# Kernel optimization log

Measured on AMD Instinct MI355X. Metric: run time of the kernel, lower is better.

Reference implementation:

```python
import jax, jax.numpy as jnp
import numpy as np

D_MODEL = 1024
NUM_HEADS = 16
DEPTH = D_MODEL // NUM_HEADS
B, S = 2, 2048


def setup_inputs() -> dict:
    key = jax.random.key(0)
    ks = jax.random.split(key, 12)
    scale = 1.0 / np.sqrt(D_MODEL)
    inp = {
        "Q": jax.random.normal(ks[0], (B, S, D_MODEL), jnp.float32),
        "K": jax.random.normal(ks[1], (B, S, D_MODEL), jnp.float32),
        "V": jax.random.normal(ks[2], (B, S, D_MODEL), jnp.float32),
        # causal mask: 1 where attention is disallowed (strictly upper triangular)
        "mask": jnp.triu(jnp.ones((1, 1, S, S), jnp.float32), k=1),
        "Wq": jax.random.normal(ks[3], (D_MODEL, D_MODEL), jnp.float32) * scale,
        "bq": jnp.zeros((D_MODEL,), jnp.float32),
        "Wk": jax.random.normal(ks[4], (D_MODEL, D_MODEL), jnp.float32) * scale,
        "bk": jnp.zeros((D_MODEL,), jnp.float32),
        "Wv": jax.random.normal(ks[5], (D_MODEL, D_MODEL), jnp.float32) * scale,
        "bv": jnp.zeros((D_MODEL,), jnp.float32),
        "Wo": jax.random.normal(ks[6], (D_MODEL, D_MODEL), jnp.float32) * scale,
        "bo": jnp.zeros((D_MODEL,), jnp.float32),
    }
    return inp


def _split_heads(x):
    # [B, S, d_model] -> [B, H, S, depth]
    b, s, _ = x.shape
    return x.reshape(b, s, NUM_HEADS, DEPTH).transpose(0, 2, 1, 3)


def reference(Q, K, V, mask, Wq, bq, Wk, bk, Wv, bv, Wo, bo):
    q = _split_heads(Q @ Wq + bq)  # [B,H,S,depth]
    k = _split_heads(K @ Wk + bk)
    v = _split_heads(V @ Wv + bv)

    scale = 1.0 / jnp.sqrt(jnp.asarray(DEPTH, q.dtype))
    scores = jnp.einsum("bhqd,bhkd->bhqk", q, k) * scale
    scores = scores + mask * (-1e9)
    attn = jax.nn.softmax(scores, axis=-1)  # [B,H,S,S]
    ctx = jnp.einsum("bhqk,bhkd->bhqd", attn, v)

    # combine heads: [B,H,S,depth] -> [B,S,d_model]
    ctx = ctx.transpose(0, 2, 1, 3).reshape(Q.shape[0], -1, D_MODEL)
    out = ctx @ Wo + bo
    return out, attn
```

## Files before the change

kernel.cpp:

```cpp
#include <hip/hip_runtime.h>
#include <hip/hip_bf16.h>
#include <cstdint>
#include <cstddef>


typedef __bf16 bf16x8 __attribute__((ext_vector_type(8)));
typedef float  f32x4  __attribute__((ext_vector_type(4)));
typedef short  short8 __attribute__((ext_vector_type(8)));
typedef unsigned short u16;
typedef unsigned int   u32;

using gas_p = const __attribute__((address_space(1))) void*;
using las_p = __attribute__((address_space(3))) void*;

static __device__ __forceinline__ u16 f2bf(float x) {
    unsigned u = __builtin_bit_cast(unsigned, x);
    u += 0x7FFFu + ((u >> 16) & 1u);
    return (u16)(u >> 16);
}
static __device__ __forceinline__ u32 pk2(float a, float b) {
    return (u32)f2bf(a) | ((u32)f2bf(b) << 16);
}
static __device__ __forceinline__ f32x4 mfma16(bf16x8 a, bf16x8 b, f32x4 c) {
    return __builtin_amdgcn_mfma_f32_16x16x32_bf16(a, b, c, 0, 0, 0);
}
static __device__ __forceinline__ bf16x8 ldb8(const u16* p) {
    return *reinterpret_cast<const bf16x8*>(p);
}

__global__ __launch_bounds__(256) void cvt_bf16_k(const float* __restrict__ Q,
                                                  const float* __restrict__ K,
                                                  const float* __restrict__ V,
                                                  u16* __restrict__ Qb,
                                                  u16* __restrict__ Kb,
                                                  u16* __restrict__ Vb) {
    const int z = blockIdx.y;
    const float* in = (z == 0) ? Q : (z == 1) ? K : V;
    u16* out = (z == 0) ? Qb : (z == 1) ? Kb : Vb;
    size_t i = (size_t)blockIdx.x * 256 + threadIdx.x;
    const float4* p = reinterpret_cast<const float4*>(in) + 2 * i;
    float4 a = p[0], b = p[1];
    short8 r;
    r[0] = (short)f2bf(a.x); r[1] = (short)f2bf(a.y);
    r[2] = (short)f2bf(a.z); r[3] = (short)f2bf(a.w);
    r[4] = (short)f2bf(b.x); r[5] = (short)f2bf(b.y);
    r[6] = (short)f2bf(b.z); r[7] = (short)f2bf(b.w);
    *reinterpret_cast<short8*>(out + 8 * i) = r;
}

__global__ __launch_bounds__(256) void transpose_cvt_k(const float* __restrict__ Wq,
                                                       const float* __restrict__ Wk,
                                                       const float* __restrict__ Wv,
                                                       const float* __restrict__ Wo,
                                                       u16* __restrict__ Wt3,
                                                       u16* __restrict__ Wto) {
    const int z = blockIdx.z;
    const float* in = (z == 0) ? Wq : (z == 1) ? Wk : (z == 2) ? Wv : Wo;
    u16* out = (z < 3) ? (Wt3 + (size_t)z * 1048576) : Wto;
    __shared__ float t[32][33];
    const int tx = threadIdx.x, ty = threadIdx.y;
    const int x  = blockIdx.x * 32 + tx;
    const int y0 = blockIdx.y * 32 + ty;
#pragma unroll
    for (int j = 0; j < 32; j += 8)
        t[ty + j][tx] = in[(size_t)(y0 + j) * 1024 + x];
    __syncthreads();
    const int x2 = blockIdx.y * 32 + tx;
    const int y2 = blockIdx.x * 32 + ty;
#pragma unroll
    for (int j = 0; j < 32; j += 8)
        out[(size_t)(y2 + j) * 1024 + x2] = f2bf(t[tx][ty + j]);
}

__global__ __launch_bounds__(256) void gemm_qkv_k(const u16* __restrict__ Qb,
                                                  const u16* __restrict__ Kb,
                                                  const u16* __restrict__ Vb,
                                                  const u16* __restrict__ Wt3,
                                                  const float* __restrict__ bq,
                                                  const float* __restrict__ bk,
                                                  const float* __restrict__ bv,
                                                  u16* __restrict__ qf,
                                                  u16* __restrict__ kf,
                                                  u16* __restrict__ vtf) {
    constexpr int Kd = 1024;
    const int z = blockIdx.z;
    const u16* A  = (z == 0) ? Qb : (z == 1) ? Kb : Vb;
    const u16* Bt = Wt3 + (size_t)z * 1048576;
    const float* bias = (z == 0) ? bq : (z == 1) ? bk : bv;

    __shared__ __align__(16) u16 As[128 * 64];
    __shared__ __align__(16) u16 Bs[128 * 64];
    const int tid = threadIdx.x;
    const int w = tid >> 6, lane = tid & 63;
    const int g = lane >> 4, lr = lane & 15;
    const int wr = w >> 1, wc = w & 1;
    const int bm = blockIdx.y * 128, bn = blockIdx.x * 128;

    f32x4 acc[4][4];
#pragma unroll
    for (int a = 0; a < 4; ++a)
#pragma unroll
        for (int b = 0; b < 4; ++b) acc[a][b] = f32x4{0.f, 0.f, 0.f, 0.f};

    for (int kt = 0; kt < Kd; kt += 64) {
#pragma unroll
        for (int it = 0; it < 4; ++it) {
            const int t2  = it * 256 + tid;
            const int row = t2 >> 3, ch = t2 & 7;
            const int ub  = (it * 256 + w * 64) * 8;
            __builtin_amdgcn_global_load_lds(
                (gas_p)(A + (size_t)(bm + row) * Kd + kt + ch * 8),
                (las_p)(As + ub), 16, 0, 0);
            __builtin_amdgcn_global_load_lds(
                (gas_p)(Bt + (size_t)(bn + row) * Kd + kt + ch * 8),
                (las_p)(Bs + ub), 16, 0, 0);
        }
        __syncthreads();
#pragma unroll
        for (int kk = 0; kk < 2; ++kk) {
            bf16x8 af[4], bfv[4];
#pragma unroll
            for (int mi = 0; mi < 4; ++mi)
                af[mi] = ldb8(As + (wr * 64 + mi * 16 + lr) * 64 + kk * 32 + g * 8);
#pragma unroll
            for (int ni = 0; ni < 4; ++ni)
                bfv[ni] = ldb8(Bs + (wc * 64 + ni * 16 + lr) * 64 + kk * 32 + g * 8);
#pragma unroll
            for (int mi = 0; mi < 4; ++mi)
#pragma unroll
                for (int ni = 0; ni < 4; ++ni)
                    acc[mi][ni] = mfma16(af[mi], bfv[ni], acc[mi][ni]);
        }
        __syncthreads();
    }

#pragma unroll
    for (int ni = 0; ni < 4; ++ni) {
        const int col = bn + wc * 64 + ni * 16 + lr;
        const float bvv = bias[col];
#pragma unroll
        for (int mi = 0; mi < 4; ++mi) {
            const int row0 = bm + wr * 64 + mi * 16 + g * 4;
            f32x4 c = acc[mi][ni];
            if (z == 2) {
                const int b = row0 >> 11, s0 = row0 & 2047;
                const int h = col >> 6,  d = col & 63;
                ushort4 pk;
                pk.x = f2bf(c[0] + bvv); pk.y = f2bf(c[1] + bvv);
                pk.z = f2bf(c[2] + bvv); pk.w = f2bf(c[3] + bvv);
                *reinterpret_cast<ushort4*>(
                    vtf + ((size_t)(b * 16 + h) * 64 + d) * 2048 + s0) = pk;
            } else {
#pragma unroll
                for (int i = 0; i < 4; ++i) {
                    const int row = row0 + i;
                    const int b = row >> 11, s = row & 2047;
                    const int h = col >> 6,  d = col & 63;
                    u16* dst = (z == 0) ? qf : kf;
                    dst[((size_t)(b * 16 + h) * 2048 + s) * 64 + d] =
                        f2bf(c[i] + bvv);
                }
            }
        }
    }
}

__global__ __launch_bounds__(256) void gemm_out_k(const u16* __restrict__ A,
                                                  const u16* __restrict__ Bt,
                                                  const float* __restrict__ bias,
                                                  float* __restrict__ dst) {
    constexpr int Kd = 1024;
    __shared__ __align__(16) u16 As[128 * 64];
    __shared__ __align__(16) u16 Bs[128 * 64];
    const int tid = threadIdx.x;
    const int w = tid >> 6, lane = tid & 63;
    const int g = lane >> 4, lr = lane & 15;
    const int wr = w >> 1, wc = w & 1;
    const int bm = blockIdx.y * 128, bn = blockIdx.x * 128;

    f32x4 acc[4][4];
#pragma unroll
    for (int a = 0; a < 4; ++a)
#pragma unroll
        for (int b = 0; b < 4; ++b) acc[a][b] = f32x4{0.f, 0.f, 0.f, 0.f};

    for (int kt = 0; kt < Kd; kt += 64) {
#pragma unroll
        for (int it = 0; it < 4; ++it) {
            const int t2  = it * 256 + tid;
            const int row = t2 >> 3, ch = t2 & 7;
            const int ub  = (it * 256 + w * 64) * 8;
            __builtin_amdgcn_global_load_lds(
                (gas_p)(A + (size_t)(bm + row) * Kd + kt + ch * 8),
                (las_p)(As + ub), 16, 0, 0);
            __builtin_amdgcn_global_load_lds(
                (gas_p)(Bt + (size_t)(bn + row) * Kd + kt + ch * 8),
                (las_p)(Bs + ub), 16, 0, 0);
        }
        __syncthreads();
#pragma unroll
        for (int kk = 0; kk < 2; ++kk) {
            bf16x8 af[4], bfv[4];
#pragma unroll
            for (int mi = 0; mi < 4; ++mi)
                af[mi] = ldb8(As + (wr * 64 + mi * 16 + lr) * 64 + kk * 32 + g * 8);
#pragma unroll
            for (int ni = 0; ni < 4; ++ni)
                bfv[ni] = ldb8(Bs + (wc * 64 + ni * 16 + lr) * 64 + kk * 32 + g * 8);
#pragma unroll
            for (int mi = 0; mi < 4; ++mi)
#pragma unroll
                for (int ni = 0; ni < 4; ++ni)
                    acc[mi][ni] = mfma16(af[mi], bfv[ni], acc[mi][ni]);
        }
        __syncthreads();
    }

#pragma unroll
    for (int ni = 0; ni < 4; ++ni) {
        const int col = bn + wc * 64 + ni * 16 + lr;
        const float bvv = bias[col];
#pragma unroll
        for (int mi = 0; mi < 4; ++mi) {
            const int row0 = bm + wr * 64 + mi * 16 + g * 4;
            f32x4 c = acc[mi][ni];
#pragma unroll
            for (int i = 0; i < 4; ++i)
                dst[(size_t)(row0 + i) * 1024 + col] = c[i] + bvv;
        }
    }
}

__global__ __launch_bounds__(256) void attn_fused_k(const u16* __restrict__ qbuf,
                                                    const u16* __restrict__ kbuf,
                                                    const u16* __restrict__ vtbuf,
                                                    float* __restrict__ attn,
                                                    u16* __restrict__ ctx) {
    constexpr int S = 2048;
    constexpr float SC2 = 0.125f * 1.44269504088896340736f;
    const int bh = blockIdx.y;
    const int pr = blockIdx.x;
    const int tid = threadIdx.x;
    const int w = tid >> 6, lane = tid & 63, g = lane >> 4, lr = lane & 15;

    const u16* qh = qbuf + (size_t)bh * S * 64;
    const u16* kh = kbuf + (size_t)bh * S * 64;
    const u16* vh = vtbuf + (size_t)bh * 64 * S;
    float* attn_h = attn + (size_t)bh * S * S;

    __shared__ __align__(16) u16 Ks[2][64 * 64];
    __shared__ __align__(16) u16 Vs[2][64 * 64];
    __shared__ __align__(16) u16 P[4][2][16][72];

    const int srow8 = lane >> 3;
    const int scol  = ((lane & 7) ^ srow8) * 8;
    const int swq   = (lr & 7) << 3;
    const int b = bh >> 4, h = bh & 15;

    for (int phase = 0; phase < 2; ++phase) {
        const int j  = phase ? (31 - pr) : pr;
        const int nT = j + 1;
        const int qb = j * 64 + w * 16;
        const int qrow = qb + lr;

        const u16* qp = qh + (size_t)qrow * 64;
        const bf16x8 q0 = ldb8(qp + g * 8);
        const bf16x8 q1 = ldb8(qp + 32 + g * 8);

        float m2 = -1e30f, l = 0.f;
#pragma unroll
        for (int ii = 0; ii < 2; ++ii) {
            const int i = w * 2 + ii, row = i * 8 + srow8;
            __builtin_amdgcn_global_load_lds(
                (gas_p)(kh + (size_t)row * 64 + scol),
                (las_p)(Ks[0] + i * 512), 16, 0, 0);
        }
        __syncthreads();
        for (int t = 0; t < nT; ++t) {
            const int cur = t & 1;
            if (t + 1 < nT) {
#pragma unroll
                for (int ii = 0; ii < 2; ++ii) {
                    const int i = w * 2 + ii;
                    const int row = (t + 1) * 64 + i * 8 + srow8;
                    __builtin_amdgcn_global_load_lds(
                        (gas_p)(kh + (size_t)row * 64 + scol),
                        (las_p)(Ks[cur ^ 1] + i * 512), 16, 0, 0);
                }
            }
            const int kc = t * 64;
            f32x4 c[4];
#pragma unroll
            for (int n = 0; n < 4; ++n) {
                const u16* kr = Ks[cur] + (n * 16 + lr) * 64;
                f32x4 z4 = {0.f, 0.f, 0.f, 0.f};
                z4   = mfma16(ldb8(kr + ((g * 8) ^ swq)), q0, z4);
                c[n] = mfma16(ldb8(kr + ((32 + g * 8) ^ swq)), q1, z4);
            }
            float xm = -__builtin_inff();
#pragma unroll
            for (int n = 0; n < 4; ++n)
#pragma unroll
                for (int i = 0; i < 4; ++i) {
                    const int kcol = kc + n * 16 + g * 4 + i;
                    const float v = (kcol <= qrow) ? c[n][i] * SC2 : -__builtin_inff();
                    c[n][i] = v;
                    xm = fmaxf(xm, v);
                }
            xm = fmaxf(xm, __shfl_xor(xm, 16));
            xm = fmaxf(xm, __shfl_xor(xm, 32));
            const float mn = fmaxf(m2, xm);
            float sum = 0.f;
#pragma unroll
            for (int n = 0; n < 4; ++n)
#pragma unroll
                for (int i = 0; i < 4; ++i) sum += exp2f(c[n][i] - mn);
            sum += __shfl_xor(sum, 16);
            sum += __shfl_xor(sum, 32);
            l = l * exp2f(m2 - mn) + sum;
            m2 = mn;
            __syncthreads();
        }
        const float invl = 1.f / l;

        f32x4 acc[4];
#pragma unroll
        for (int dn = 0; dn < 4; ++dn) acc[dn] = f32x4{0.f, 0.f, 0.f, 0.f};

#pragma unroll
        for (int ii = 0; ii < 2; ++ii) {
            const int i = w * 2 + ii, row = i * 8 + srow8;
            __builtin_amdgcn_global_load_lds(
                (gas_p)(kh + (size_t)row * 64 + scol),
                (las_p)(Ks[0] + i * 512), 16, 0, 0);
            __builtin_amdgcn_global_load_lds(
                (gas_p)(vh + (size_t)row * 2048 + scol),
                (las_p)(Vs[0] + i * 512), 16, 0, 0);
        }
        __syncthreads();
        for (int t = 0; t < nT; ++t) {
            const int cur = t & 1;
            if (t + 1 < nT) {
#pragma unroll
                for (int ii = 0; ii < 2; ++ii) {
                    const int i = w * 2 + ii;
                    const int krow = (t + 1) * 64 + i * 8 + srow8;
                    const int vrow = i * 8 + srow8;
                    __builtin_amdgcn_global_load_lds(
                        (gas_p)(kh + (size_t)krow * 64 + scol),
                        (las_p)(Ks[cur ^ 1] + i * 512), 16, 0, 0);
                    __builtin_amdgcn_global_load_lds(
                        (gas_p)(vh + (size_t)vrow * 2048 + (t + 1) * 64 + scol),
                        (las_p)(Vs[cur ^ 1] + i * 512), 16, 0, 0);
                }
            }
            const int kc = t * 64;
            f32x4 c[4];
#pragma unroll
            for (int n = 0; n < 4; ++n) {
                const u16* kr = Ks[cur] + (n * 16 + lr) * 64;
                f32x4 z4 = {0.f, 0.f, 0.f, 0.f};
                z4   = mfma16(ldb8(kr + ((g * 8) ^ swq)), q0, z4);
                c[n] = mfma16(ldb8(kr + ((32 + g * 8) ^ swq)), q1, z4);
            }
#pragma unroll
            for (int n = 0; n < 4; ++n) {
                f32x4 pv;
#pragma unroll
                for (int i = 0; i < 4; ++i) {
                    const int kcol = kc + n * 16 + g * 4 + i;
                    pv[i] = (kcol <= qrow) ? exp2f(c[n][i] * SC2 - m2) * invl : 0.f;
                }
                *reinterpret_cast<f32x4*>(attn_h + (size_t)qrow * S + kc + n * 16 + g * 4) = pv;
                uint2 pr2;
                pr2.x = pk2(pv[0], pv[1]);
                pr2.y = pk2(pv[2], pv[3]);
                *reinterpret_cast<uint2*>(&P[w][t & 1][lr][n * 16 + g * 4]) = pr2;
            }
            asm volatile("s_waitcnt lgkmcnt(0)" ::: "memory");
            __builtin_amdgcn_sched_barrier(0);
#pragma unroll
            for (int kk = 0; kk < 2; ++kk) {
                const bf16x8 pa = ldb8(&P[w][t & 1][lr][kk * 32 + g * 8]);
#pragma unroll
                for (int dn = 0; dn < 4; ++dn) {
                    const u16* vr = Vs[cur] + (dn * 16 + lr) * 64;
                    acc[dn] = mfma16(pa, ldb8(vr + ((kk * 32 + g * 8) ^ swq)), acc[dn]);
                }
            }
            __syncthreads();
        }

#pragma unroll
        for (int dn = 0; dn < 4; ++dn)
#pragma unroll
            for (int i = 0; i < 4; ++i) {
                const size_t row = (size_t)b * S + qb + g * 4 + i;
                ctx[row * 1024 + h * 64 + dn * 16 + lr] = f2bf(acc[dn][i]);
            }

        const int z0 = nT * 64;
        const f32x4 zz = {0.f, 0.f, 0.f, 0.f};
        float* rowp = attn_h + (size_t)qrow * S;
        for (int c0 = z0 + g * 4; c0 < S; c0 += 16)
            *reinterpret_cast<f32x4*>(rowp + c0) = zz;
        __syncthreads();
    }
}

extern "C" void kernel_launch(void* const* d_in, const int* in_sizes, int n_in,
                              void* d_out, int out_size, void* d_ws, size_t ws_size,
                              hipStream_t stream) {
    (void)in_sizes; (void)n_in; (void)out_size; (void)ws_size;

    const float* Q  = (const float*)d_in[0];
    const float* K  = (const float*)d_in[1];
    const float* V  = (const float*)d_in[2];
    const float* Wq = (const float*)d_in[4];
    const float* bq = (const float*)d_in[5];
    const float* Wk = (const float*)d_in[6];
    const float* bk = (const float*)d_in[7];
    const float* Wv = (const float*)d_in[8];
    const float* bv = (const float*)d_in[9];
    const float* Wo = (const float*)d_in[10];
    const float* bo = (const float*)d_in[11];

    char* ws = (char*)d_ws;
    u16* Qb  = (u16*)(ws);
    u16* Kb  = (u16*)(ws + ((size_t)8  << 20));
    u16* Vb  = (u16*)(ws + ((size_t)16 << 20));
    u16* Wt3 = (u16*)(ws + ((size_t)24 << 20));
    u16* Wto = (u16*)(ws + ((size_t)30 << 20));
    u16* qf  = (u16*)(ws + ((size_t)32 << 20));
    u16* kf  = (u16*)(ws + ((size_t)40 << 20));
    u16* vtf = (u16*)(ws + ((size_t)48 << 20));
    u16* ctx = (u16*)(ws + ((size_t)56 << 20));

    float* out  = (float*)d_out;
    float* attn = out + (size_t)4096 * 1024;

    cvt_bf16_k<<<dim3(2048, 3), 256, 0, stream>>>(Q, K, V, Qb, Kb, Vb);

    transpose_cvt_k<<<dim3(32, 32, 4), dim3(32, 8), 0, stream>>>(Wq, Wk, Wv, Wo, Wt3, Wto);

    gemm_qkv_k<<<dim3(8, 32, 3), 256, 0, stream>>>(Qb, Kb, Vb, Wt3, bq, bk, bv, qf, kf, vtf);

    attn_fused_k<<<dim3(16, 32), 256, 0, stream>>>(qf, kf, vtf, attn, ctx);

    gemm_out_k<<<dim3(8, 32), 256, 0, stream>>>(ctx, Wto, bo, out);
}
```

Before: 297.5 us.

## Move causal-mask zero fill into QKV GEMM and relax attention loop barriers

Zeroing the upper-triangular part of the attention matrix moves out of the attention kernel into an extra z-slice of the QKV projection GEMM launch. Those streaming stores can then overlap with GEMM compute instead of lengthening the attention tail. The attention loops also replace full __syncthreads with explicit vmcnt waits plus s_barrier, and skip the barrier on the last tile, to trim synchronisation cost. The vmcnt(4) count in the second loop depends on exact counting of outstanding loads. The extra zero-fill blocks may be imbalanced, since c runs up to 31.

```diff
diff --git a/kernel.cpp b/kernel.cpp
--- a/kernel.cpp
+++ b/kernel.cpp
@@ -81,9 +81,26 @@
                                                   const float* __restrict__ bv,
                                                   u16* __restrict__ qf,
                                                   u16* __restrict__ kf,
-                                                  u16* __restrict__ vtf) {
+                                                  u16* __restrict__ vtf,
+                                                  float* __restrict__ attn) {
     constexpr int Kd = 1024;
+    constexpr int S = 2048;
     const int z = blockIdx.z;
+
+    if (z == 3) {
+        float* attn_h = attn + (size_t)blockIdx.y * S * S;
+        const int bx = blockIdx.x;
+        const int ro = threadIdx.x >> 4, cc = threadIdx.x & 15;
+        const f32x4 zz = {0.f, 0.f, 0.f, 0.f};
+        for (int c = 1; c < 32; ++c) {
+            float* base = attn_h + (size_t)(bx * 8 * c) * S + c * 64 + cc * 4;
+            const int nrows = 8 * c;
+            for (int i = ro; i < nrows; i += 16)
+                *reinterpret_cast<f32x4*>(base + (size_t)i * S) = zz;
+        }
+        return;
+    }
+
     const u16* A  = (z == 0) ? Qb : (z == 1) ? Kb : Vb;
     const u16* Bt = Wt3 + (size_t)z * 1048576;
     const float* bias = (z == 0) ? bq : (z == 1) ? bk : bv;
@@ -287,6 +304,7 @@
                         (gas_p)(kh + (size_t)row * 64 + scol),
                         (las_p)(Ks[cur ^ 1] + i * 512), 16, 0, 0);
                 }
+                __builtin_amdgcn_sched_barrier(0);
             }
             const int kc = t * 64;
             f32x4 c[4];
@@ -319,7 +337,11 @@
             sum += __shfl_xor(sum, 32);
             l = l * exp2f(m2 - mn) + sum;
             m2 = mn;
-            __syncthreads();
+            if (t + 1 < nT) {
+                asm volatile("s_waitcnt vmcnt(0)" ::: "memory");
+                __builtin_amdgcn_s_barrier();
+                __builtin_amdgcn_sched_barrier(0);
+            }
         }
         const float invl = 1.f / l;
 
@@ -327,6 +349,7 @@
 #pragma unroll
         for (int dn = 0; dn < 4; ++dn) acc[dn] = f32x4{0.f, 0.f, 0.f, 0.f};
 
+        __syncthreads();
 #pragma unroll
         for (int ii = 0; ii < 2; ++ii) {
             const int i = w * 2 + ii, row = i * 8 + srow8;
@@ -353,6 +376,7 @@
                         (gas_p)(vh + (size_t)vrow * 2048 + (t + 1) * 64 + scol),
                         (las_p)(Vs[cur ^ 1] + i * 512), 16, 0, 0);
                 }
+                __builtin_amdgcn_sched_barrier(0);
             }
             const int kc = t * 64;
             f32x4 c[4];
@@ -388,7 +412,11 @@
                     acc[dn] = mfma16(pa, ldb8(vr + ((kk * 32 + g * 8) ^ swq)), acc[dn]);
                 }
             }
-            __syncthreads();
+            if (t + 1 < nT) {
+                asm volatile("s_waitcnt vmcnt(4)" ::: "memory");
+                __builtin_amdgcn_s_barrier();
+                __builtin_amdgcn_sched_barrier(0);
+            }
         }
 
 #pragma unroll
@@ -398,12 +426,6 @@
                 const size_t row = (size_t)b * S + qb + g * 4 + i;
                 ctx[row * 1024 + h * 64 + dn * 16 + lr] = f2bf(acc[dn][i]);
             }
-
-        const int z0 = nT * 64;
-        const f32x4 zz = {0.f, 0.f, 0.f, 0.f};
-        float* rowp = attn_h + (size_t)qrow * S;
-        for (int c0 = z0 + g * 4; c0 < S; c0 += 16)
-            *reinterpret_cast<f32x4*>(rowp + c0) = zz;
         __syncthreads();
     }
 }
@@ -443,7 +465,8 @@
 
     transpose_cvt_k<<<dim3(32, 32, 4), dim3(32, 8), 0, stream>>>(Wq, Wk, Wv, Wo, Wt3, Wto);
 
-    gemm_qkv_k<<<dim3(8, 32, 3), 256, 0, stream>>>(Qb, Kb, Vb, Wt3, bq, bk, bv, qf, kf, vtf);
+    gemm_qkv_k<<<dim3(8, 32, 4), 256, 0, stream>>>(Qb, Kb, Vb, Wt3, bq, bk, bv,
+                                                   qf, kf, vtf, attn);
 
     attn_fused_k<<<dim3(16, 32), 256, 0, stream>>>(qf, kf, vtf, attn, ctx);
 
```

Result: no change. 291.6 us (-2.0%).
